# Optimization experiments

Hardware: AMD Instinct MI355X
Metric: run time of the kernel (lower is better)

Reference implementation:

```python
import jax, jax.numpy as jnp
import numpy as np

N_CENTER, N_NEAR, N_STEPK, N_HOPS = 512, 32, 10, 2
FEAT_NAMES = ["xyz_fea", "pmt_fea", "mad_fea", "dim_fea", "nor_fea", "loc_fea", "fea"]


def pairwise_sqdist(x):
    # x: [B,N,C] -> [B,N,N]
    xx = jnp.sum(x * x, axis=-1)
    return xx[:, :, None] + xx[:, None, :] - 2.0 * jnp.einsum('bnc,bmc->bnm', x, x)


def surface_knn(x, n_near, n_stepk, n_hops=N_HOPS):
    # Iterative surface-KNN: build a step-KNN graph with n_stepk neighbors,
    # expand the neighborhood n_hops times (neighbor-of-neighbor union), then
    # pick the n_near nearest points among the reachable candidate set.
    d = pairwise_sqdist(x)                      # [B,N,N]
    B, N, _ = d.shape
    _, nbr = jax.lax.top_k(-d, n_stepk + 1)     # step neighbors (incl. self)
    b_idx = jnp.arange(B)[:, None, None]
    r_idx = jnp.arange(N)[None, :, None]
    adj = jnp.zeros((B, N, N), jnp.bool_).at[b_idx, r_idx, nbr].set(True)
    reach = adj
    adj_f = adj.astype(jnp.float32)
    for _ in range(n_hops):
        reach = (jnp.einsum('bij,bjk->bik', reach.astype(jnp.float32), adj_f) > 0) | adj
    dm = jnp.where(reach, d, jnp.inf)
    _, idx = jax.lax.top_k(-dm, n_near)         # [B,N,n_near], nearest reachable
    return idx


def fps(x, n_center):
    # Farthest point sampling in the C-dim feature space (dim=dim in source).
    B, N, _ = x.shape
    d = pairwise_sqdist(x)
    barange = jnp.arange(B)

    def step(carry, _):
        mind, prev = carry
        mind = jnp.minimum(mind, d[barange, prev])   # [B,N]
        nxt = jnp.argmax(mind, axis=-1).astype(jnp.int32)
        return (mind, nxt), nxt

    init = (jnp.full((B, N), jnp.inf, jnp.float32), jnp.zeros((B,), jnp.int32))
    _, rest = jax.lax.scan(step, init, None, length=n_center - 1)  # [S-1,B]
    idx = jnp.concatenate([jnp.zeros((1, B), jnp.int32), rest], axis=0)
    return idx.T                                   # [B,S]


def branch(center, grouped, wq, bq, wk, bk, wv, bv, w1, b1, w2, b2):
    # center: [B,S,C], grouped: [B,S,K,C]
    C = center.shape[-1]
    q = center @ wq + bq                           # [B,S,C]
    k = grouped @ wk + bk                          # [B,S,K,C]
    v = grouped @ wv + bv
    scores = jnp.einsum('bsc,bskc->bsk', q, k) / jnp.sqrt(jnp.float32(C))
    attn = jax.nn.softmax(scores, axis=-1)
    out = jnp.einsum('bsk,bskc->bsc', attn, v)     # attention pooling -> [B,S,C]
    h = jax.nn.relu(out @ w1 + b1)                 # MLP (C -> Cout -> Cout)
    return jax.nn.relu(h @ w2 + b2)


def setup_inputs() -> dict:
    key = jax.random.key(0)
    ks = jax.random.split(key, 16)
    B, N, C, CO = 8, 2048, 128, 256
    inp = {}
    for i, name in enumerate(FEAT_NAMES):
        inp[name] = jax.random.normal(ks[i], (B, N, C), jnp.float32)
    s = np.float32(1.0 / np.sqrt(C))
    so = np.float32(1.0 / np.sqrt(CO))
    inp['aw_q'] = jax.random.normal(ks[7], (7, C, C), jnp.float32) * s
    inp['ab_q'] = jnp.zeros((7, C), jnp.float32)
    inp['aw_k'] = jax.random.normal(ks[8], (7, C, C), jnp.float32) * s
    inp['ab_k'] = jnp.zeros((7, C), jnp.float32)
    inp['aw_v'] = jax.random.normal(ks[9], (7, C, C), jnp.float32) * s
    inp['ab_v'] = jnp.zeros((7, C), jnp.float32)
    inp['mw1'] = jax.random.normal(ks[10], (7, C, CO), jnp.float32) * s
    inp['mb1'] = jnp.zeros((7, CO), jnp.float32)
    inp['mw2'] = jax.random.normal(ks[11], (7, CO, CO), jnp.float32) * so
    inp['mb2'] = jnp.zeros((7, CO), jnp.float32)
    return inp


def reference(xyz_fea, pmt_fea, mad_fea, dim_fea, nor_fea, loc_fea, fea,
              aw_q, ab_q, aw_k, ab_k, aw_v, ab_v, mw1, mb1, mw2, mb2):
    B = xyz_fea.shape[0]
    feats = jnp.stack([xyz_fea, pmt_fea, mad_fea, dim_fea, nor_fea, loc_fea, fea], 0)  # [7,B,N,C]
    idx_all = surface_knn(xyz_fea, N_NEAR, N_STEPK)      # [B,N,K]
    fps_idx = fps(xyz_fea, N_CENTER)                     # [B,S]
    b2 = jnp.arange(B)[:, None]                          # [B,1]
    b3 = jnp.arange(B)[:, None, None]                    # [B,1,1]
    centers = feats[:, b2, fps_idx]                      # [7,B,S,C]
    idx = idx_all[b2, fps_idx]                           # [B,S,K]
    grouped = feats[:, b3, idx]                          # [7,B,S,K,C]
    outs = jax.vmap(branch)(centers, grouped, aw_q, ab_q, aw_k, ab_k,
                            aw_v, ab_v, mw1, mb1, mw2, mb2)  # [7,B,S,CO]
    return tuple(outs[i] for i in range(7))
```

## Files before the change

kernel.cpp:

```cpp
#include <hip/hip_runtime.h>
#include <hip/hip_bf16.h>
#include <math.h>

constexpr int BATCH = 8;
constexpr int NPTS  = 2048;
constexpr int CH    = 128;
constexpr int CHO   = 256;
constexpr int NCEN  = 512;
constexpr int NNEI  = 32;
constexpr int NTOP  = 11;
constexpr int NW    = 64;
constexpr int SMEM_BYTES = 17408;
constexpr int SMEM_MID   = 20608;

struct Ptr7 { const float* p[7]; };

__global__ __launch_bounds__(256) void xx_kernel(const float* __restrict__ x,
                                                 float* __restrict__ xx) {
    int p = blockIdx.x * 256 + threadIdx.x;
    if (p >= BATCH * NPTS) return;
    const float4* xr = (const float4*)(x + (size_t)p * CH);
    float s = 0.f;
#pragma unroll
    for (int i = 0; i < CH / 4; i++) {
        float4 v = xr[i];
        s += v.x * v.x + v.y * v.y + v.z * v.z + v.w * v.w;
    }
    xx[p] = s;
}

__global__ __launch_bounds__(256) void dmat_kernel(const float* __restrict__ x,
                                                   const float* __restrict__ xx,
                                                   float* __restrict__ D) {
    __shared__ __align__(16) char smem[SMEM_BYTES];
    int it = blockIdx.y, jt = blockIdx.x;
    if (jt < it) return;
    float (*As)[68] = (float(*)[68])smem;
    float (*Bs)[68] = (float(*)[68])(smem + 32 * 68 * 4);
    int bz = blockIdx.z;
    int i0 = it * 64, j0 = jt * 64;
    const float* X = x + (size_t)bz * NPTS * CH;
    int t = threadIdx.x, tx = t & 15, ty = t >> 4;
    int lr = t >> 3, lc = (t & 7) * 4;
    const float* ai0 = X + (size_t)(i0 + lr) * CH;
    const float* ai1 = X + (size_t)(i0 + lr + 32) * CH;
    const float* bj0 = X + (size_t)(j0 + lr) * CH;
    const float* bj1 = X + (size_t)(j0 + lr + 32) * CH;
    float acc[4][4] = {};
    for (int kc = 0; kc < CH; kc += 32) {
        float4 a0 = *(const float4*)(ai0 + kc + lc);
        float4 a1 = *(const float4*)(ai1 + kc + lc);
        float4 b0 = *(const float4*)(bj0 + kc + lc);
        float4 b1 = *(const float4*)(bj1 + kc + lc);
        __syncthreads();
        As[lc + 0][lr] = a0.x; As[lc + 1][lr] = a0.y; As[lc + 2][lr] = a0.z; As[lc + 3][lr] = a0.w;
        As[lc + 0][lr + 32] = a1.x; As[lc + 1][lr + 32] = a1.y; As[lc + 2][lr + 32] = a1.z; As[lc + 3][lr + 32] = a1.w;
        Bs[lc + 0][lr] = b0.x; Bs[lc + 1][lr] = b0.y; Bs[lc + 2][lr] = b0.z; Bs[lc + 3][lr] = b0.w;
        Bs[lc + 0][lr + 32] = b1.x; Bs[lc + 1][lr + 32] = b1.y; Bs[lc + 2][lr + 32] = b1.z; Bs[lc + 3][lr + 32] = b1.w;
        __syncthreads();
#pragma unroll
        for (int kk = 0; kk < 32; kk++) {
            float4 av = *(const float4*)&As[kk][ty * 4];
            float4 bv = *(const float4*)&Bs[kk][tx * 4];
            float a[4] = {av.x, av.y, av.z, av.w};
            float b[4] = {bv.x, bv.y, bv.z, bv.w};
#pragma unroll
            for (int i = 0; i < 4; i++)
#pragma unroll
                for (int j = 0; j < 4; j++) acc[i][j] += a[i] * b[j];
        }
    }
    const float* xxb = xx + bz * NPTS;
    float xi[4], xj[4];
#pragma unroll
    for (int i = 0; i < 4; i++) xi[i] = xxb[i0 + ty * 4 + i];
#pragma unroll
    for (int j = 0; j < 4; j++) xj[j] = xxb[j0 + tx * 4 + j];
    float ov[4][4];
#pragma unroll
    for (int i = 0; i < 4; i++)
#pragma unroll
        for (int j = 0; j < 4; j++) ov[i][j] = xi[i] + xj[j] - 2.f * acc[i][j];
#pragma unroll
    for (int i = 0; i < 4; i++) {
        float4 o = {ov[i][0], ov[i][1], ov[i][2], ov[i][3]};
        *(float4*)(D + ((size_t)bz * NPTS + i0 + ty * 4 + i) * NPTS + j0 + tx * 4) = o;
    }
    if (jt > it) {
        __syncthreads();
        float (*T)[65] = (float(*)[65])smem;
#pragma unroll
        for (int i = 0; i < 4; i++)
#pragma unroll
            for (int j = 0; j < 4; j++) T[ty * 4 + i][tx * 4 + j] = ov[i][j];
        __syncthreads();
#pragma unroll
        for (int i = 0; i < 4; i++) {
            float4 o;
            o.x = T[tx * 4 + 0][ty * 4 + i];
            o.y = T[tx * 4 + 1][ty * 4 + i];
            o.z = T[tx * 4 + 2][ty * 4 + i];
            o.w = T[tx * 4 + 3][ty * 4 + i];
            *(float4*)(D + ((size_t)bz * NPTS + j0 + ty * 4 + i) * NPTS + i0 + tx * 4) = o;
        }
    }
}

__global__ __launch_bounds__(256) void fused_front_kernel(const float* __restrict__ D,
                                                          unsigned int* __restrict__ adj,
                                                          int* __restrict__ fps_idx) {
    __shared__ __align__(16) char smem[SMEM_BYTES];
    if (blockIdx.x < BATCH) {
        int lane = threadIdx.x;
        if (lane >= 64) return;
        int b = blockIdx.x;
        float4* mp = (float4*)smem;
        float4 inf4 = {INFINITY, INFINITY, INFINITY, INFINITY};
#pragma unroll
        for (int k = 0; k < 8; k++) mp[lane + 64 * k] = inf4;
        int prev = 0;
        if (lane == 0) fps_idx[b * NCEN] = 0;
        const float* Db = D + (size_t)b * NPTS * NPTS;
        for (int s = 1; s < NCEN; s++) {
            const float4* rowp = (const float4*)(Db + (size_t)prev * NPTS);
            float4 g0 = rowp[lane + 0 * 64];
            float4 g1 = rowp[lane + 1 * 64];
            float4 g2 = rowp[lane + 2 * 64];
            float4 g3 = rowp[lane + 3 * 64];
            float4 g4 = rowp[lane + 4 * 64];
            float4 g5 = rowp[lane + 5 * 64];
            float4 g6 = rowp[lane + 6 * 64];
            float4 g7 = rowp[lane + 7 * 64];
            float4 gg[8] = {g0, g1, g2, g3, g4, g5, g6, g7};
            float bv = -INFINITY; int bj = NPTS;
#pragma unroll
            for (int k = 0; k < 8; k++) {
                int li = lane + 64 * k;
                float4 m = mp[li];
                m.x = fminf(m.x, gg[k].x);
                m.y = fminf(m.y, gg[k].y);
                m.z = fminf(m.z, gg[k].z);
                m.w = fminf(m.w, gg[k].w);
                mp[li] = m;
                int j0 = 4 * li;
                if (m.x > bv) { bv = m.x; bj = j0 + 0; }
                if (m.y > bv) { bv = m.y; bj = j0 + 1; }
                if (m.z > bv) { bv = m.z; bj = j0 + 2; }
                if (m.w > bv) { bv = m.w; bj = j0 + 3; }
            }
#pragma unroll
            for (int off = 32; off > 0; off >>= 1) {
                float ov = __shfl_xor(bv, off);
                int oj = __shfl_xor(bj, off);
                if (ov > bv || (ov == bv && oj < bj)) { bv = ov; bj = oj; }
            }
            if (lane == 0) fps_idx[b * NCEN + s] = bj;
            prev = bj;
        }
        return;
    }
    float* row = (float*)smem;
    float* rv = row + NPTS;
    int* ri = (int*)(rv + 256);
    int* picks = ri + 256;
    int rid = blockIdx.x - BATCH;
    const float* Dr = D + (size_t)rid * NPTS;
    int t = threadIdx.x;
    float4* rp = (float4*)row;
    rp[t] = ((const float4*)Dr)[t];
    rp[t + 256] = ((const float4*)Dr)[t + 256];
    __syncthreads();
    for (int it = 0; it < NTOP; it++) {
        float bv = row[t];
        int bi = t;
#pragma unroll
        for (int k = 1; k < 8; k++) {
            int j = t + (k << 8);
            float v = row[j];
            if (v < bv) { bv = v; bi = j; }
        }
        rv[t] = bv; ri[t] = bi;
        __syncthreads();
        for (int off = 128; off > 0; off >>= 1) {
            if (t < off) {
                float ovv = rv[t + off]; int oi = ri[t + off];
                if (ovv < rv[t] || (ovv == rv[t] && oi < ri[t])) { rv[t] = ovv; ri[t] = oi; }
            }
            __syncthreads();
        }
        if (t == 0) { picks[it] = ri[0]; row[ri[0]] = INFINITY; }
        __syncthreads();
    }
    if (t < NW) {
        unsigned w = 0;
#pragma unroll
        for (int p = 0; p < NTOP; p++) {
            int j = picks[p];
            if ((j >> 5) == t) w |= 1u << (j & 31);
        }
        adj[(size_t)rid * NW + t] = w;
    }
}

__global__ void make_gather(const int* __restrict__ fps_idx, int* __restrict__ gatherC) {
    int r = blockIdx.x * 256 + threadIdx.x;
    if (r >= BATCH * NCEN) return;
    int b = r >> 9, s = r & 511;
    gatherC[r] = b * NPTS + fps_idx[b * NCEN + s];
}

template <int KSIZE, bool RELU>
__device__ __forceinline__ void gemm_tile64(char* smem,
                                            const float* __restrict__ A, int lda,
                                            const int* __restrict__ gather,
                                            const float* __restrict__ W, int ldw,
                                            const float* __restrict__ bias,
                                            float* __restrict__ Out, int ldo) {
    float (*As)[68] = (float(*)[68])smem;
    float (*Ws)[68] = (float(*)[68])(smem + 32 * 68 * 4);
    int t = threadIdx.x;
    int tx = t & 15, ty = t >> 4;
    int lr = t >> 3, lc = (t & 7) * 4;
    const float* ar0 = A + (size_t)(gather ? gather[lr] : lr) * lda;
    const float* ar1 = A + (size_t)(gather ? gather[lr + 32] : lr + 32) * lda;
    float acc[4][4] = {};
    for (int kc = 0; kc < KSIZE; kc += 32) {
        float4 a0 = *(const float4*)(ar0 + kc + lc);
        float4 a1 = *(const float4*)(ar1 + kc + lc);
        float4 w0 = *(const float4*)(W + (size_t)(kc + lr) * ldw + lc);
        float4 w1 = *(const float4*)(W + (size_t)(kc + lr) * ldw + lc + 32);
        __syncthreads();
        As[lc + 0][lr] = a0.x; As[lc + 1][lr] = a0.y; As[lc + 2][lr] = a0.z; As[lc + 3][lr] = a0.w;
        As[lc + 0][lr + 32] = a1.x; As[lc + 1][lr + 32] = a1.y; As[lc + 2][lr + 32] = a1.z; As[lc + 3][lr + 32] = a1.w;
        *(float4*)&Ws[lr][lc] = w0;
        *(float4*)&Ws[lr][lc + 32] = w1;
        __syncthreads();
#pragma unroll
        for (int kk = 0; kk < 32; kk++) {
            float4 av = *(const float4*)&As[kk][ty * 4];
            float4 wv = *(const float4*)&Ws[kk][tx * 4];
            float a[4] = {av.x, av.y, av.z, av.w};
            float w[4] = {wv.x, wv.y, wv.z, wv.w};
#pragma unroll
            for (int i = 0; i < 4; i++)
#pragma unroll
                for (int j = 0; j < 4; j++) acc[i][j] += a[i] * w[j];
        }
    }
#pragma unroll
    for (int i = 0; i < 4; i++) {
        int r = ty * 4 + i;
        float4 o;
        o.x = acc[i][0] + bias[tx * 4 + 0];
        o.y = acc[i][1] + bias[tx * 4 + 1];
        o.z = acc[i][2] + bias[tx * 4 + 2];
        o.w = acc[i][3] + bias[tx * 4 + 3];
        if (RELU) {
            o.x = fmaxf(o.x, 0.f); o.y = fmaxf(o.y, 0.f);
            o.z = fmaxf(o.z, 0.f); o.w = fmaxf(o.w, 0.f);
        }
        *(float4*)(Out + (size_t)r * ldo + tx * 4) = o;
    }
}

__global__ __launch_bounds__(256) void fused_mid_kernel(const unsigned int* __restrict__ adj,
                                                        const float* __restrict__ D,
                                                        const int* __restrict__ fps_idx,
                                                        int* __restrict__ idx_sel,
                                                        Ptr7 feats,
                                                        const float* __restrict__ awq,
                                                        const float* __restrict__ abq,
                                                        const int* __restrict__ gatherC,
                                                        float* __restrict__ qtab) {
    __shared__ __align__(16) char smem[SMEM_MID];
    if (blockIdx.x >= NCEN * BATCH) {
        int id = blockIdx.x - NCEN * BATCH;
        int rt = id & 63;
        int ct = (id >> 6) & 1;
        int v = id >> 7;
        gemm_tile64<CH, false>(smem, feats.p[v], CH, gatherC + rt * 64,
                               awq + (size_t)v * CH * CH + ct * 64, CH,
                               abq + v * CH + ct * 64,
                               qtab + ((size_t)v * (BATCH * NCEN) + rt * 64) * CH + ct * 64, CH);
        return;
    }
    unsigned* adjw = (unsigned*)smem;
    unsigned* R1 = adjw + NW;
    unsigned* R2 = R1 + NW;
    int* cnt = (int*)(R2 + NW);
    int* lst = (int*)(smem + 1024);
    float* dst = (float*)(smem + 1024 + 8192);
    int* sel = (int*)(smem + 1024 + 16384);
    int s = blockIdx.x & (NCEN - 1), b = blockIdx.x >> 9, t = threadIdx.x;
    int i = fps_idx[b * NCEN + s];
    const unsigned* arow = adj + ((size_t)(b * NPTS + i)) * NW;
    if (t < NW) { adjw[t] = arow[t]; R1[t] = arow[t]; }
    if (t == 0) cnt[0] = 0;
    __syncthreads();
    if (t < NW) {
        unsigned w = adjw[t];
        while (w) { int bb = __ffs(w) - 1; w &= w - 1; int p = atomicAdd(cnt, 1); lst[p] = t * 32 + bb; }
    }
    __syncthreads();
    int n1 = cnt[0];
    {
        int g = t >> 6, lane = t & 63;
        for (int p = g; p < n1; p += 4) {
            unsigned aw = adj[((size_t)(b * NPTS + lst[p])) * NW + lane];
            atomicOr(&R1[lane], aw);
        }
    }
    __syncthreads();
    if (t == 0) cnt[0] = 0;
    __syncthreads();
    if (t < NW) {
        unsigned w = R1[t];
        while (w) { int bb = __ffs(w) - 1; w &= w - 1; int p = atomicAdd(cnt, 1); lst[p] = t * 32 + bb; }
        R2[t] = adjw[t];
    }
    __syncthreads();
    int n2 = cnt[0];
    {
        int g = t >> 6, lane = t & 63;
        for (int p = g; p < n2; p += 4) {
            unsigned aw = adj[((size_t)(b * NPTS + lst[p])) * NW + lane];
            atomicOr(&R2[lane], aw);
        }
    }
    __syncthreads();
    if (t == 0) cnt[0] = 0;
    __syncthreads();
    const float* Dr = D + (size_t)(b * NPTS + i) * NPTS;
    if (t < NW) {
        unsigned w = R2[t];
        while (w) {
            int bb = __ffs(w) - 1; w &= w - 1;
            int j = t * 32 + bb;
            int p = atomicAdd(cnt, 1);
            lst[p] = j; dst[p] = Dr[j];
        }
    }
    __syncthreads();
    if (t >= 64) return;
    int L = cnt[0];
    int nsel = L < NNEI ? L : NNEI;
    int lane = t;
    for (int r = 0; r < nsel; r++) {
        float bv = INFINITY; int bj = 0x7fffffff, bp = -1;
        for (int p = lane; p < L; p += 64) {
            float v = dst[p]; int j = lst[p];
            if (v < bv || (v == bv && j < bj)) { bv = v; bj = j; bp = p; }
        }
#pragma unroll
        for (int off = 32; off > 0; off >>= 1) {
            float ov = __shfl_xor(bv, off);
            int oj = __shfl_xor(bj, off);
            int op = __shfl_xor(bp, off);
            if (ov < bv || (ov == bv && oj < bj)) { bv = ov; bj = oj; bp = op; }
        }
        if (lane == 0) { sel[r] = bj; dst[bp] = INFINITY; }
    }
    if (lane == 0 && nsel < NNEI) {
        int r = nsel;
        for (int j = 0; j < NPTS && r < NNEI; j++)
            if (!((R2[j >> 5] >> (j & 31)) & 1)) sel[r++] = j;
    }
    if (lane < NNEI) idx_sel[((size_t)(b * NCEN + s)) * NNEI + lane] = sel[lane];
}

__global__ __launch_bounds__(256) void kvproj_kernel(Ptr7 feats, const float* __restrict__ awk,
                                                     const float* __restrict__ abk,
                                                     const float* __restrict__ awv,
                                                     const float* __restrict__ abv,
                                                     float* __restrict__ ktab,
                                                     float* __restrict__ vtab) {
    __shared__ __align__(16) char smem[SMEM_BYTES];
    int v = blockIdx.z, ct = blockIdx.y, rt = blockIdx.x;
    bool isv = ct >= 2;
    int c2 = ct & 1;
    const float* A = feats.p[v] + (size_t)rt * 64 * CH;
    const float* W = (isv ? awv : awk) + (size_t)v * CH * CH + c2 * 64;
    const float* bias = (isv ? abv : abk) + v * CH + c2 * 64;
    float* Out = (isv ? vtab : ktab) + (size_t)v * (BATCH * NPTS) * CH + (size_t)rt * 64 * CH + c2 * 64;
    gemm_tile64<CH, false>(smem, A, CH, nullptr, W, CH, bias, Out, CH);
}

__global__ __launch_bounds__(256) void mlp1_kernel(const float* __restrict__ otab,
                                                   const float* __restrict__ mw1,
                                                   const float* __restrict__ mb1,
                                                   float* __restrict__ htab) {
    __shared__ __align__(16) char smem[SMEM_BYTES];
    int v = blockIdx.z, ct = blockIdx.y, rt = blockIdx.x;
    gemm_tile64<CH, true>(smem, otab + ((size_t)v * (BATCH * NCEN) + rt * 64) * CH, CH, nullptr,
                          mw1 + (size_t)v * CH * CHO + ct * 64, CHO,
                          mb1 + v * CHO + ct * 64,
                          htab + ((size_t)v * (BATCH * NCEN) + rt * 64) * CHO + ct * 64, CHO);
}

__global__ __launch_bounds__(256) void mlp2_kernel(const float* __restrict__ htab,
                                                   const float* __restrict__ mw2,
                                                   const float* __restrict__ mb2,
                                                   float* __restrict__ out) {
    __shared__ __align__(16) char smem[SMEM_BYTES];
    int v = blockIdx.z, ct = blockIdx.y, rt = blockIdx.x;
    gemm_tile64<CHO, true>(smem, htab + ((size_t)v * (BATCH * NCEN) + rt * 64) * CHO, CHO, nullptr,
                           mw2 + (size_t)v * CHO * CHO + ct * 64, CHO,
                           mb2 + v * CHO + ct * 64,
                           out + ((size_t)v * (BATCH * NCEN) + rt * 64) * CHO + ct * 64, CHO);
}

__global__ __launch_bounds__(256) void attn_kernel(const float* __restrict__ qtab,
                                                   const float* __restrict__ ktab,
                                                   const float* __restrict__ vtab,
                                                   const int* __restrict__ idx_sel,
                                                   float* __restrict__ otab) {
    __shared__ float q_s[4][CH];
    __shared__ float attn_s[4][NNEI];
    __shared__ int jj_s[4][NNEI];
    int v = blockIdx.y;
    int t = threadIdx.x, w = t >> 6, lane = t & 63;
    int cg = blockIdx.x * 4 + w;
    int b = cg >> 9, s = cg & 511;
    const float* qr = qtab + ((size_t)v * (BATCH * NCEN) + cg) * CH;
    *(float2*)&q_s[w][lane * 2] = *(const float2*)(qr + lane * 2);
    if (lane < NNEI) jj_s[w][lane] = idx_sel[((size_t)(b * NCEN + s)) * NNEI + lane];
    __syncthreads();
    if (lane < NNEI) {
        int j = jj_s[w][lane];
        const float* kr = ktab + ((size_t)v * (BATCH * NPTS) + b * NPTS + j) * CH;
        float acc = 0.f;
#pragma unroll
        for (int c4 = 0; c4 < CH / 4; c4++) {
            float4 qv = *(const float4*)&q_s[w][c4 * 4];
            float4 kv = *(const float4*)(kr + c4 * 4);
            acc += qv.x * kv.x + qv.y * kv.y + qv.z * kv.z + qv.w * kv.w;
        }
        float sc = acc * 0.08838834764831845f;
        float m = sc;
#pragma unroll
        for (int off = 16; off > 0; off >>= 1) m = fmaxf(m, __shfl_xor(m, off, 32));
        float e = expf(sc - m);
        float sum = e;
#pragma unroll
        for (int off = 16; off > 0; off >>= 1) sum += __shfl_xor(sum, off, 32);
        attn_s[w][lane] = e / sum;
    }
    __syncthreads();
    float2 o = {0.f, 0.f};
    const float* vbase = vtab + ((size_t)v * (BATCH * NPTS) + b * NPTS) * CH;
    for (int tt = 0; tt < NNEI; tt++) {
        int j = jj_s[w][tt];
        float a = attn_s[w][tt];
        float2 vv = *(const float2*)(vbase + (size_t)j * CH + lane * 2);
        o.x += a * vv.x;
        o.y += a * vv.y;
    }
    *(float2*)(otab + ((size_t)v * (BATCH * NCEN) + cg) * CH + lane * 2) = o;
}

extern "C" void kernel_launch(void* const* d_in, const int* in_sizes, int n_in,
                              void* d_out, int out_size, void* d_ws, size_t ws_size,
                              hipStream_t stream) {
    (void)in_sizes; (void)n_in; (void)out_size;
    Ptr7 feats;
    for (int i = 0; i < 7; i++) feats.p[i] = (const float*)d_in[i];
    const float* awq = (const float*)d_in[7];
    const float* abq = (const float*)d_in[8];
    const float* awk = (const float*)d_in[9];
    const float* abk = (const float*)d_in[10];
    const float* awv = (const float*)d_in[11];
    const float* abv = (const float*)d_in[12];
    const float* mw1 = (const float*)d_in[13];
    const float* mb1 = (const float*)d_in[14];
    const float* mw2 = (const float*)d_in[15];
    const float* mb2 = (const float*)d_in[16];
    const float* xyz = feats.p[0];

    char* ws = (char*)d_ws;
    size_t SZ_D = (size_t)BATCH * NPTS * NPTS * 4;
    float* D = (float*)ws;
    float* ktab = (float*)ws;
    float* vtab = (float*)(ws + (size_t)7 * BATCH * NPTS * CH * 4);
    size_t off = SZ_D;
    float* xx = (float*)(ws + off); off += (size_t)BATCH * NPTS * 4;
    unsigned* adjb = (unsigned*)(ws + off); off += (size_t)BATCH * NPTS * NW * 4;
    int* fpsidx = (int*)(ws + off); off += (size_t)BATCH * NCEN * 4;
    int* idxsel = (int*)(ws + off); off += (size_t)BATCH * NCEN * NNEI * 4;
    int* gatherC = (int*)(ws + off); off += (size_t)BATCH * NCEN * 4;
    float* qtab = (float*)(ws + off); off += (size_t)7 * BATCH * NCEN * CH * 4;
    float* otab = (float*)(ws + off); off += (size_t)7 * BATCH * NCEN * CH * 4;
    float* htab = (float*)(ws + off); off += (size_t)7 * BATCH * NCEN * CHO * 4;
    if (ws_size < off) return;

    xx_kernel<<<dim3((BATCH * NPTS + 255) / 256), dim3(256), 0, stream>>>(xyz, xx);
    dmat_kernel<<<dim3(NPTS / 64, NPTS / 64, BATCH), dim3(256), 0, stream>>>(xyz, xx, D);
    fused_front_kernel<<<dim3(BATCH + BATCH * NPTS), dim3(256), 0, stream>>>(D, adjb, fpsidx);
    make_gather<<<dim3((BATCH * NCEN + 255) / 256), dim3(256), 0, stream>>>(fpsidx, gatherC);
    fused_mid_kernel<<<dim3(NCEN * BATCH + 2 * 7 * (BATCH * NCEN / 64)), dim3(256), 0, stream>>>(
        adjb, D, fpsidx, idxsel, feats, awq, abq, gatherC, qtab);
    kvproj_kernel<<<dim3(BATCH * NPTS / 64, 4, 7), dim3(256), 0, stream>>>(feats, awk, abk, awv, abv, ktab, vtab);
    attn_kernel<<<dim3(BATCH * NCEN / 4, 7), dim3(256), 0, stream>>>(qtab, ktab, vtab, idxsel, otab);
    mlp1_kernel<<<dim3(BATCH * NCEN / 64, 4, 7), dim3(256), 0, stream>>>(otab, mw1, mb1, htab);
    mlp2_kernel<<<dim3(BATCH * NCEN / 64, 4, 7), dim3(256), 0, stream>>>(htab, mw2, mb2, (float*)d_out);
}
```

Before: 1.132 ms.

## Overlap K projection with serial FPS by fusing it into front kernel

Moves the K-projection GEMM tiles into the fused front kernel as extra blocks, so they run alongside the long serial FPS blocks and the KNN row blocks instead of in a later kernel. To make this legal, ktab is relocated out of the D region, which is still live at that point, whenever the workspace is large enough. The layout is reshuffled so vtab, htab and otab reuse the D region afterwards. A fallback keeps the old combined KV projection when the workspace is too small, which adds branching and buffer-aliasing complexity.

```diff
diff --git a/kernel.cpp b/kernel.cpp
--- a/kernel.cpp
+++ b/kernel.cpp
@@ -106,109 +106,6 @@
     }
 }
 
-__global__ __launch_bounds__(256) void fused_front_kernel(const float* __restrict__ D,
-                                                          unsigned int* __restrict__ adj,
-                                                          int* __restrict__ fps_idx) {
-    __shared__ __align__(16) char smem[SMEM_BYTES];
-    if (blockIdx.x < BATCH) {
-        int lane = threadIdx.x;
-        if (lane >= 64) return;
-        int b = blockIdx.x;
-        float4* mp = (float4*)smem;
-        float4 inf4 = {INFINITY, INFINITY, INFINITY, INFINITY};
-#pragma unroll
-        for (int k = 0; k < 8; k++) mp[lane + 64 * k] = inf4;
-        int prev = 0;
-        if (lane == 0) fps_idx[b * NCEN] = 0;
-        const float* Db = D + (size_t)b * NPTS * NPTS;
-        for (int s = 1; s < NCEN; s++) {
-            const float4* rowp = (const float4*)(Db + (size_t)prev * NPTS);
-            float4 g0 = rowp[lane + 0 * 64];
-            float4 g1 = rowp[lane + 1 * 64];
-            float4 g2 = rowp[lane + 2 * 64];
-            float4 g3 = rowp[lane + 3 * 64];
-            float4 g4 = rowp[lane + 4 * 64];
-            float4 g5 = rowp[lane + 5 * 64];
-            float4 g6 = rowp[lane + 6 * 64];
-            float4 g7 = rowp[lane + 7 * 64];
-            float4 gg[8] = {g0, g1, g2, g3, g4, g5, g6, g7};
-            float bv = -INFINITY; int bj = NPTS;
-#pragma unroll
-            for (int k = 0; k < 8; k++) {
-                int li = lane + 64 * k;
-                float4 m = mp[li];
-                m.x = fminf(m.x, gg[k].x);
-                m.y = fminf(m.y, gg[k].y);
-                m.z = fminf(m.z, gg[k].z);
-                m.w = fminf(m.w, gg[k].w);
-                mp[li] = m;
-                int j0 = 4 * li;
-                if (m.x > bv) { bv = m.x; bj = j0 + 0; }
-                if (m.y > bv) { bv = m.y; bj = j0 + 1; }
-                if (m.z > bv) { bv = m.z; bj = j0 + 2; }
-                if (m.w > bv) { bv = m.w; bj = j0 + 3; }
-            }
-#pragma unroll
-            for (int off = 32; off > 0; off >>= 1) {
-                float ov = __shfl_xor(bv, off);
-                int oj = __shfl_xor(bj, off);
-                if (ov > bv || (ov == bv && oj < bj)) { bv = ov; bj = oj; }
-            }
-            if (lane == 0) fps_idx[b * NCEN + s] = bj;
-            prev = bj;
-        }
-        return;
-    }
-    float* row = (float*)smem;
-    float* rv = row + NPTS;
-    int* ri = (int*)(rv + 256);
-    int* picks = ri + 256;
-    int rid = blockIdx.x - BATCH;
-    const float* Dr = D + (size_t)rid * NPTS;
-    int t = threadIdx.x;
-    float4* rp = (float4*)row;
-    rp[t] = ((const float4*)Dr)[t];
-    rp[t + 256] = ((const float4*)Dr)[t + 256];
-    __syncthreads();
-    for (int it = 0; it < NTOP; it++) {
-        float bv = row[t];
-        int bi = t;
-#pragma unroll
-        for (int k = 1; k < 8; k++) {
-            int j = t + (k << 8);
-            float v = row[j];
-            if (v < bv) { bv = v; bi = j; }
-        }
-        rv[t] = bv; ri[t] = bi;
-        __syncthreads();
-        for (int off = 128; off > 0; off >>= 1) {
-            if (t < off) {
-                float ovv = rv[t + off]; int oi = ri[t + off];
-                if (ovv < rv[t] || (ovv == rv[t] && oi < ri[t])) { rv[t] = ovv; ri[t] = oi; }
-            }
-            __syncthreads();
-        }
-        if (t == 0) { picks[it] = ri[0]; row[ri[0]] = INFINITY; }
-        __syncthreads();
-    }
-    if (t < NW) {
-        unsigned w = 0;
-#pragma unroll
-        for (int p = 0; p < NTOP; p++) {
-            int j = picks[p];
-            if ((j >> 5) == t) w |= 1u << (j & 31);
-        }
-        adj[(size_t)rid * NW + t] = w;
-    }
-}
-
-__global__ void make_gather(const int* __restrict__ fps_idx, int* __restrict__ gatherC) {
-    int r = blockIdx.x * 256 + threadIdx.x;
-    if (r >= BATCH * NCEN) return;
-    int b = r >> 9, s = r & 511;
-    gatherC[r] = b * NPTS + fps_idx[b * NCEN + s];
-}
-
 template <int KSIZE, bool RELU>
 __device__ __forceinline__ void gemm_tile64(char* smem,
                                             const float* __restrict__ A, int lda,
@@ -263,6 +160,127 @@
     }
 }
 
+__global__ __launch_bounds__(256) void fused_front_kernel(const float* __restrict__ D,
+                                                          unsigned int* __restrict__ adj,
+                                                          int* __restrict__ fps_idx,
+                                                          Ptr7 feats,
+                                                          const float* __restrict__ awk,
+                                                          const float* __restrict__ abk,
+                                                          float* __restrict__ ktab) {
+    __shared__ __align__(16) char smem[SMEM_BYTES];
+    if (blockIdx.x < BATCH) {
+        int lane = threadIdx.x;
+        if (lane >= 64) return;
+        int b = blockIdx.x;
+        float4* mp = (float4*)smem;
+        float4 inf4 = {INFINITY, INFINITY, INFINITY, INFINITY};
+#pragma unroll
+        for (int k = 0; k < 8; k++) mp[lane + 64 * k] = inf4;
+        int prev = 0;
+        if (lane == 0) fps_idx[b * NCEN] = 0;
+        const float* Db = D + (size_t)b * NPTS * NPTS;
+        for (int s = 1; s < NCEN; s++) {
+            const float4* rowp = (const float4*)(Db + (size_t)prev * NPTS);
+            float4 g0 = rowp[lane + 0 * 64];
+            float4 g1 = rowp[lane + 1 * 64];
+            float4 g2 = rowp[lane + 2 * 64];
+            float4 g3 = rowp[lane + 3 * 64];
+            float4 g4 = rowp[lane + 4 * 64];
+            float4 g5 = rowp[lane + 5 * 64];
+            float4 g6 = rowp[lane + 6 * 64];
+            float4 g7 = rowp[lane + 7 * 64];
+            float4 gg[8] = {g0, g1, g2, g3, g4, g5, g6, g7};
+            float bv = -INFINITY; int bj = NPTS;
+#pragma unroll
+            for (int k = 0; k < 8; k++) {
+                int li = lane + 64 * k;
+                float4 m = mp[li];
+                m.x = fminf(m.x, gg[k].x);
+                m.y = fminf(m.y, gg[k].y);
+                m.z = fminf(m.z, gg[k].z);
+                m.w = fminf(m.w, gg[k].w);
+                mp[li] = m;
+                int j0 = 4 * li;
+                if (m.x > bv) { bv = m.x; bj = j0 + 0; }
+                if (m.y > bv) { bv = m.y; bj = j0 + 1; }
+                if (m.z > bv) { bv = m.z; bj = j0 + 2; }
+                if (m.w > bv) { bv = m.w; bj = j0 + 3; }
+            }
+#pragma unroll
+            for (int off = 32; off > 0; off >>= 1) {
+                float ov = __shfl_xor(bv, off);
+                int oj = __shfl_xor(bj, off);
+                if (ov > bv || (ov == bv && oj < bj)) { bv = ov; bj = oj; }
+            }
+            if (lane == 0) fps_idx[b * NCEN + s] = bj;
+            prev = bj;
+        }
+        return;
+    }
+    if (blockIdx.x < BATCH + BATCH * NPTS) {
+        float* row = (float*)smem;
+        float* rv = row + NPTS;
+        int* ri = (int*)(rv + 256);
+        int* picks = ri + 256;
+        int rid = blockIdx.x - BATCH;
+        const float* Dr = D + (size_t)rid * NPTS;
+        int t = threadIdx.x;
+        float4* rp = (float4*)row;
+        rp[t] = ((const float4*)Dr)[t];
+        rp[t + 256] = ((const float4*)Dr)[t + 256];
+        __syncthreads();
+        for (int it = 0; it < NTOP; it++) {
+            float bv = row[t];
+            int bi = t;
+#pragma unroll
+            for (int k = 1; k < 8; k++) {
+                int j = t + (k << 8);
+                float v = row[j];
+                if (v < bv) { bv = v; bi = j; }
+            }
+            rv[t] = bv; ri[t] = bi;
+            __syncthreads();
+            for (int off = 128; off > 0; off >>= 1) {
+                if (t < off) {
+                    float ovv = rv[t + off]; int oi = ri[t + off];
+                    if (ovv < rv[t] || (ovv == rv[t] && oi < ri[t])) { rv[t] = ovv; ri[t] = oi; }
+                }
+                __syncthreads();
+            }
+            if (t == 0) { picks[it] = ri[0]; row[ri[0]] = INFINITY; }
+            __syncthreads();
+        }
+        if (t < NW) {
+            unsigned w = 0;
+#pragma unroll
+            for (int p = 0; p < NTOP; p++) {
+                int j = picks[p];
+                if ((j >> 5) == t) w |= 1u << (j & 31);
+            }
+            adj[(size_t)rid * NW + t] = w;
+        }
+        return;
+    }
+    {
+        int id = blockIdx.x - BATCH - BATCH * NPTS;
+        int rt = id & 255;
+        int c2 = (id >> 8) & 1;
+        int v = id >> 9;
+        const float* A = feats.p[v] + (size_t)rt * 64 * CH;
+        const float* W = awk + (size_t)v * CH * CH + c2 * 64;
+        const float* bias = abk + v * CH + c2 * 64;
+        float* Out = ktab + (size_t)v * (BATCH * NPTS) * CH + (size_t)rt * 64 * CH + c2 * 64;
+        gemm_tile64<CH, false>(smem, A, CH, nullptr, W, CH, bias, Out, CH);
+    }
+}
+
+__global__ void make_gather(const int* __restrict__ fps_idx, int* __restrict__ gatherC) {
+    int r = blockIdx.x * 256 + threadIdx.x;
+    if (r >= BATCH * NCEN) return;
+    int b = r >> 9, s = r & 511;
+    gatherC[r] = b * NPTS + fps_idx[b * NCEN + s];
+}
+
 __global__ __launch_bounds__(256) void fused_mid_kernel(const unsigned int* __restrict__ adj,
                                                         const float* __restrict__ D,
                                                         const int* __restrict__ fps_idx,
@@ -385,6 +403,19 @@
     gemm_tile64<CH, false>(smem, A, CH, nullptr, W, CH, bias, Out, CH);
 }
 
+__global__ __launch_bounds__(256) void vproj_kernel(Ptr7 feats,
+                                                    const float* __restrict__ awv,
+                                                    const float* __restrict__ abv,
+                                                    float* __restrict__ vtab) {
+    __shared__ __align__(16) char smem[SMEM_BYTES];
+    int v = blockIdx.z, c2 = blockIdx.y, rt = blockIdx.x;
+    const float* A = feats.p[v] + (size_t)rt * 64 * CH;
+    const float* W = awv + (size_t)v * CH * CH + c2 * 64;
+    const float* bias = abv + v * CH + c2 * 64;
+    float* Out = vtab + (size_t)v * (BATCH * NPTS) * CH + (size_t)rt * 64 * CH + c2 * 64;
+    gemm_tile64<CH, false>(smem, A, CH, nullptr, W, CH, bias, Out, CH);
+}
+
 __global__ __launch_bounds__(256) void mlp1_kernel(const float* __restrict__ otab,
                                                    const float* __restrict__ mw1,
                                                    const float* __restrict__ mb1,
@@ -478,27 +509,47 @@
 
     char* ws = (char*)d_ws;
     size_t SZ_D = (size_t)BATCH * NPTS * NPTS * 4;
+    size_t SZ_KV = (size_t)7 * BATCH * NPTS * CH * 4;
+    size_t SZ_Q  = (size_t)7 * BATCH * NCEN * CH * 4;
+    size_t SZ_O  = SZ_Q;
+    size_t SZ_H  = (size_t)7 * BATCH * NCEN * CHO * 4;
     float* D = (float*)ws;
-    float* ktab = (float*)ws;
-    float* vtab = (float*)(ws + (size_t)7 * BATCH * NPTS * CH * 4);
     size_t off = SZ_D;
     float* xx = (float*)(ws + off); off += (size_t)BATCH * NPTS * 4;
     unsigned* adjb = (unsigned*)(ws + off); off += (size_t)BATCH * NPTS * NW * 4;
     int* fpsidx = (int*)(ws + off); off += (size_t)BATCH * NCEN * 4;
     int* idxsel = (int*)(ws + off); off += (size_t)BATCH * NCEN * NNEI * 4;
     int* gatherC = (int*)(ws + off); off += (size_t)BATCH * NCEN * 4;
-    float* qtab = (float*)(ws + off); off += (size_t)7 * BATCH * NCEN * CH * 4;
-    float* otab = (float*)(ws + off); off += (size_t)7 * BATCH * NCEN * CH * 4;
-    float* htab = (float*)(ws + off); off += (size_t)7 * BATCH * NCEN * CHO * 4;
-    if (ws_size < off) return;
+    float* qtab = (float*)(ws + off); off += SZ_Q;
+    size_t base_off = off;
+
+    bool kv_sep = (ws_size >= base_off + SZ_KV);
+    float *ktab, *vtab, *otab, *htab;
+    if (kv_sep) {
+        ktab = (float*)(ws + base_off);
+        vtab = (float*)ws;
+        htab = (float*)(ws + SZ_KV);
+        otab = (float*)(ws + SZ_KV + SZ_H);
+    } else {
+        ktab = (float*)ws;
+        vtab = (float*)(ws + SZ_KV);
+        otab = (float*)(ws + base_off);
+        htab = (float*)(ws + base_off + SZ_O);
+        if (ws_size < base_off + SZ_O + SZ_H) return;
+    }
 
     xx_kernel<<<dim3((BATCH * NPTS + 255) / 256), dim3(256), 0, stream>>>(xyz, xx);
     dmat_kernel<<<dim3(NPTS / 64, NPTS / 64, BATCH), dim3(256), 0, stream>>>(xyz, xx, D);
-    fused_front_kernel<<<dim3(BATCH + BATCH * NPTS), dim3(256), 0, stream>>>(D, adjb, fpsidx);
+    int front_blocks = BATCH + BATCH * NPTS + (kv_sep ? 7 * 2 * 256 : 0);
+    fused_front_kernel<<<dim3(front_blocks), dim3(256), 0, stream>>>(D, adjb, fpsidx,
+                                                                     feats, awk, abk, ktab);
     make_gather<<<dim3((BATCH * NCEN + 255) / 256), dim3(256), 0, stream>>>(fpsidx, gatherC);
     fused_mid_kernel<<<dim3(NCEN * BATCH + 2 * 7 * (BATCH * NCEN / 64)), dim3(256), 0, stream>>>(
         adjb, D, fpsidx, idxsel, feats, awq, abq, gatherC, qtab);
-    kvproj_kernel<<<dim3(BATCH * NPTS / 64, 4, 7), dim3(256), 0, stream>>>(feats, awk, abk, awv, abv, ktab, vtab);
+    if (kv_sep)
+        vproj_kernel<<<dim3(BATCH * NPTS / 64, 2, 7), dim3(256), 0, stream>>>(feats, awv, abv, vtab);
+    else
+        kvproj_kernel<<<dim3(BATCH * NPTS / 64, 4, 7), dim3(256), 0, stream>>>(feats, awk, abk, awv, abv, ktab, vtab);
     attn_kernel<<<dim3(BATCH * NCEN / 4, 7), dim3(256), 0, stream>>>(qtab, ktab, vtab, idxsel, otab);
     mlp1_kernel<<<dim3(BATCH * NCEN / 64, 4, 7), dim3(256), 0, stream>>>(otab, mw1, mb1, htab);
     mlp2_kernel<<<dim3(BATCH * NCEN / 64, 4, 7), dim3(256), 0, stream>>>(htab, mw2, mb2, (float*)d_out);
```

New measurement: 1.087 ms. 4.0% less time.
